# Performance work log

Hardware: AMD Instinct MI355X
Metric: run time of the kernel (lower is better)

## Reference

```python
import jax, jax.numpy as jnp
import numpy as np

NUM_EDGE_CLASS = 4
NODE_DIM = 64
BATCH = 32
NUM_NODES = 1024


def setup_inputs() -> dict:
    key = jax.random.key(0)
    k1, k2, k3, k4, k5 = jax.random.split(key, 5)
    node_state = jax.random.normal(k1, (BATCH, NUM_NODES, NODE_DIM), dtype=jnp.float32)
    adj_mat = jax.random.randint(k2, (BATCH, NUM_NODES, NUM_NODES), 0, NUM_EDGE_CLASS, dtype=jnp.int32)
    matrix_in = jax.random.normal(k3, (NUM_EDGE_CLASS, NODE_DIM, NODE_DIM), dtype=jnp.float32) * 0.1
    matrix_out = jax.random.normal(k4, (NUM_EDGE_CLASS, NODE_DIM, NODE_DIM), dtype=jnp.float32) * 0.1
    bias = jax.random.normal(k5, (2 * NODE_DIM,), dtype=jnp.float32)
    return {"node_state": node_state, "adj_mat": adj_mat,
            "matrix_in": matrix_in, "matrix_out": matrix_out, "bias": bias}


def reference(node_state, adj_mat, matrix_in, matrix_out, bias):
    """GGNN message passing (Li et al. Eq. 2).

    Original TF code builds a [b, n*d, n*d] block matrix where block (i, j)
    is matrix_in[adj_mat[b, i, j]] (and matrix_out[adj_mat[b, j, i]] for the
    outgoing direction), then matmuls against flattened node states. The
    equivalent fused math is:
      m_in[b,i]  = sum_j matrix_in[adj[b,i,j]]  @ h[b,j]
      m_out[b,i] = sum_j matrix_out[adj[b,j,i]] @ h[b,j]
    Implemented via a one-hot over the (small) set of edge classes so the
    per-edge d x d matrices are never materialized per edge.
    """
    h = node_state  # [b, n, d]
    onehot = jax.nn.one_hot(adj_mat, NUM_EDGE_CLASS, dtype=h.dtype)  # [b, n, n, c]
    # per-class neighbor aggregation, then one small matmul per class
    s_in = jnp.einsum('bijc,bje->bice', onehot, h)          # [b, n, c, d]
    m_in = jnp.einsum('bice,cde->bid', s_in, matrix_in)      # [b, n, d]
    s_out = jnp.einsum('bjic,bje->bice', onehot, h)          # transposed adjacency
    m_out = jnp.einsum('bice,cde->bid', s_out, matrix_out)   # [b, n, d]
    message = jnp.concatenate([m_in, m_out], axis=-1) + bias  # [b, n, 2d]
    return message
```

## Files before the change

kernel.cpp:

```cpp
#include <hip/hip_runtime.h>


namespace {

typedef unsigned int  u32;
typedef unsigned short u16;
typedef __attribute__((ext_vector_type(8))) short bf16x8;
typedef __attribute__((ext_vector_type(4))) float f32x4;

constexpr int NN = 1024;
constexpr int ND = 64;

__device__ inline u16 f2bf(float x) {
    u32 u = __float_as_uint(x);
    return (u16)((u + 0x7FFFu + ((u >> 16) & 1u)) >> 16);
}
__device__ inline float bf2f(u16 x) { return __uint_as_float(((u32)x) << 16); }

__device__ inline u32 oh2(u32 z) {
    return ((z & 1u) | ((z & 4u) << 14)) * 0x3F80u;
}

__global__ __launch_bounds__(256) void pack_adjm(
    const int* __restrict__ adj, const float* __restrict__ Min,
    const float* __restrict__ Mout, u32* __restrict__ adjP,
    u32* __restrict__ adjPT, u16* __restrict__ Mws)
{
    const int t = threadIdx.x;
    const int bid = blockIdx.x;
    if (bid >= 2048) {
        for (int i = t; i < 8192; i += 256) {
            const float* M = (i < 4096) ? Min : Mout;
            int idx = i & 4095;
            float m0 = M[idx], m1 = M[4096 + idx], m2 = M[8192 + idx], m3 = M[12288 + idx];
            u16* o = Mws + (size_t)(i >> 12) * 16384;
            o[idx]         = f2bf(m1 - m0);
            o[4096 + idx]  = f2bf(m2 - m0);
            o[8192 + idx]  = f2bf(m0 - m1 - m2 + m3);
            o[12288 + idx] = f2bf(m0);
        }
        return;
    }

    __shared__ u32 rp2[16][68];
    const int b = bid >> 6, It = (bid >> 4) & 3, Jt = (bid >> 2) & 3, s = bid & 3;
    const int* base = adj + ((size_t)b << 20) + (size_t)(It * 256 + s * 64) * NN + Jt * 256;

    const int row = t >> 2, seg = t & 3;
    const int* rptr = base + (size_t)row * NN + seg * 64;
    u32 w[4];
    #pragma unroll
    for (int q = 0; q < 4; ++q) {
        int4 v0 = *(const int4*)(rptr + q * 16 + 0);
        int4 v1 = *(const int4*)(rptr + q * 16 + 4);
        int4 v2 = *(const int4*)(rptr + q * 16 + 8);
        int4 v3 = *(const int4*)(rptr + q * 16 + 12);
        u32 u = (u32)(v0.x & 3) | ((u32)(v0.y & 3) << 2) | ((u32)(v0.z & 3) << 4) | ((u32)(v0.w & 3) << 6)
              | ((u32)(v1.x & 3) << 8) | ((u32)(v1.y & 3) << 10) | ((u32)(v1.z & 3) << 12) | ((u32)(v1.w & 3) << 14)
              | ((u32)(v2.x & 3) << 16) | ((u32)(v2.y & 3) << 18) | ((u32)(v2.z & 3) << 20) | ((u32)(v2.w & 3) << 22)
              | ((u32)(v3.x & 3) << 24) | ((u32)(v3.y & 3) << 26) | ((u32)(v3.z & 3) << 28) | ((u32)(v3.w & 3) << 30);
        w[q] = u;
        rp2[seg * 4 + q][row] = u;
    }
    u32* op = adjP + (((((size_t)b * 4 + Jt) * 16 + It * 4 + s) * 4 + seg) * 64 + row) * 4;
    *(uint4*)op = make_uint4(w[0], w[1], w[2], w[3]);
    __syncthreads();

    const int sc = t >> 6, il = t & 63;
    const int cw = sc * 4 + (il >> 4);
    const int bp = (il & 15) * 2;
    u32 o[4];
    #pragma unroll
    for (int jj = 0; jj < 4; ++jj) {
        u32 r[16];
        *(uint4*)&r[0]  = *(const uint4*)&rp2[cw][jj * 16 + 0];
        *(uint4*)&r[4]  = *(const uint4*)&rp2[cw][jj * 16 + 4];
        *(uint4*)&r[8]  = *(const uint4*)&rp2[cw][jj * 16 + 8];
        *(uint4*)&r[12] = *(const uint4*)&rp2[cw][jj * 16 + 12];
        u32 acc = 0;
        #pragma unroll
        for (int k = 0; k < 16; ++k)
            acc += ((r[k] >> bp) & 3u) << (2 * k);
        o[jj] = acc;
    }
    u32* op2 = adjPT + (((((size_t)b * 4 + It) * 16 + Jt * 4 + sc) * 4 + s) * 64 + il) * 4;
    *(uint4*)op2 = make_uint4(o[0], o[1], o[2], o[3]);
}

__global__ __launch_bounds__(256) void prep_h(
    const float* __restrict__ h, u16* __restrict__ Hws, float* __restrict__ PApart)
{
    __shared__ u16 hl[256][72];
    __shared__ float red[4][64];
    const int t = threadIdx.x;
    const int b = blockIdx.x >> 2, jc = blockIdx.x & 3;
    const float* hb = h + ((size_t)b * NN + jc * 256) * ND;
    #pragma unroll
    for (int k = 0; k < 16; ++k) {
        int j = k * 16 + (t >> 4);
        int e4 = (t & 15) * 4;
        float4 v = *(const float4*)(hb + (size_t)j * ND + e4);
        *(u32*)&hl[j][e4]     = (u32)f2bf(v.x) | ((u32)f2bf(v.y) << 16);
        *(u32*)&hl[j][e4 + 2] = (u32)f2bf(v.z) | ((u32)f2bf(v.w) << 16);
    }
    __syncthreads();
    u16* ob = Hws + (size_t)(b * 4 + jc) * 2048 * 8;
    const int e = t & 63;
    float psum = 0.f;
    #pragma unroll
    for (int k = 0; k < 8; ++k) {
        int u = k * 4 + (t >> 6);
        u16 x0 = hl[u * 8 + 0][e], x1 = hl[u * 8 + 1][e], x2 = hl[u * 8 + 2][e], x3 = hl[u * 8 + 3][e];
        u16 x4 = hl[u * 8 + 4][e], x5 = hl[u * 8 + 5][e], x6 = hl[u * 8 + 6][e], x7 = hl[u * 8 + 7][e];
        psum += bf2f(x0) + bf2f(x1) + bf2f(x2) + bf2f(x3) + bf2f(x4) + bf2f(x5) + bf2f(x6) + bf2f(x7);
        u32 p0 = (u32)x0 | ((u32)x1 << 16), p1 = (u32)x2 | ((u32)x3 << 16);
        u32 p2 = (u32)x4 | ((u32)x5 << 16), p3 = (u32)x6 | ((u32)x7 << 16);
        *(uint4*)(ob + (size_t)(u * 64 + e) * 8) = make_uint4(p0, p1, p2, p3);
    }
    red[t >> 6][e] = psum;
    __syncthreads();
    if (t < 64) {
        float sum = red[0][t] + red[1][t] + red[2][t] + red[3][t];
        PApart[(size_t)(jc * 32 + b) * 64 + t] = sum;
    }
}

__global__ __launch_bounds__(256, 4) void ggnn_main(
    const u32* __restrict__ adjP, const u32* __restrict__ adjPT,
    const u16* __restrict__ Hws, const u16* __restrict__ Mws,
    const float* __restrict__ PApart, const float* __restrict__ bias,
    float* __restrict__ out)
{
    __shared__ u16 Sb[16][16][72];

    const int t = threadIdx.x;
    const int w = t >> 6;
    const int ln = t & 15, qd = (t & 63) >> 4, qd2 = qd >> 1;
    const int shamt = (qd & 1) * 16;
    const int bid = blockIdx.x;
    const int dir = bid >> 9;
    const int b = (bid >> 4) & 31, it = bid & 15;

    const u32* Adir = dir ? adjPT : adjP;
    f32x4 acc[3][4];
    #pragma unroll
    for (int p = 0; p < 3; ++p)
        #pragma unroll
        for (int nt = 0; nt < 4; ++nt) acc[p][nt] = (f32x4){0.f, 0.f, 0.f, 0.f};

    uint4 Ar[4];
    {
        const u32* at = Adir + (size_t)((b * 4 + 0) * 16 + it) * 1024;
        #pragma unroll
        for (int u = 0; u < 4; ++u)
            Ar[u] = *(const uint4*)(at + (u * 64 + w * 16 + ln) * 4);
    }

    #pragma unroll
    for (int jc = 0; jc < 4; ++jc) {
        const u16* ht = Hws + (size_t)(b * 4 + jc) * 16384;
        uint4 ArN[4];
        if (jc < 3) {
            const u32* at = Adir + (size_t)((b * 4 + jc + 1) * 16 + it) * 1024;
            #pragma unroll
            for (int u = 0; u < 4; ++u)
                ArN[u] = *(const uint4*)(at + (u * 64 + w * 16 + ln) * 4);
        }

        #pragma unroll
        for (int ks = 0; ks < 8; ++ks) {
            bf16x8 bf[4];
            #pragma unroll
            for (int nt = 0; nt < 4; ++nt)
                bf[nt] = *(const bf16x8*)(ht + (size_t)((ks * 4 + qd) * 64 + nt * 16 + ln) * 8);

            uint4 Q = Ar[ks >> 1];
            u32 a = (ks & 1) ? (qd2 ? Q.w : Q.z) : (qd2 ? Q.y : Q.x);
            u32 f = (a >> shamt) & 0xFFFFu;
            u32 x0 = f & 0x5555u;
            u32 x1 = (f >> 1) & 0x5555u;
            u32 xt = x0 & x1;

            union { u32 u[4]; bf16x8 v; } A0, A1, AT;
            #pragma unroll
            for (int wd = 0; wd < 4; ++wd) {
                A0.u[wd] = oh2(x0 >> (4 * wd));
                A1.u[wd] = oh2(x1 >> (4 * wd));
                AT.u[wd] = oh2(xt >> (4 * wd));
            }
            #pragma unroll
            for (int nt = 0; nt < 4; ++nt) {
                acc[0][nt] = __builtin_amdgcn_mfma_f32_16x16x32_bf16(A0.v, bf[nt], acc[0][nt], 0, 0, 0);
                acc[1][nt] = __builtin_amdgcn_mfma_f32_16x16x32_bf16(A1.v, bf[nt], acc[1][nt], 0, 0, 0);
                acc[2][nt] = __builtin_amdgcn_mfma_f32_16x16x32_bf16(AT.v, bf[nt], acc[2][nt], 0, 0, 0);
            }
        }
        if (jc < 3) {
            #pragma unroll
            for (int u = 0; u < 4; ++u) Ar[u] = ArN[u];
        }
    }

    #pragma unroll
    for (int p = 0; p < 3; ++p)
        #pragma unroll
        for (int nt = 0; nt < 4; ++nt)
            #pragma unroll
            for (int r = 0; r < 4; ++r)
                Sb[w * 4 + p][qd * 4 + r][nt * 16 + ln] = f2bf(acc[p][nt][r]);

    {
        const int lane64 = t & 63;
        float paf = 0.f;
        #pragma unroll
        for (int jcp = 0; jcp < 4; ++jcp)
            paf += PApart[(size_t)(jcp * 32 + b) * 64 + lane64];
        u16 pab = f2bf(paf);
        #pragma unroll
        for (int i = 0; i < 16; ++i)
            Sb[w * 4 + 3][i][lane64] = pab;
    }

    const int dofs = dir * 64;
    f32x4 acc2[4];
    #pragma unroll
    for (int dt = 0; dt < 4; ++dt) {
        float v = bias[dofs + dt * 16 + ln];
        acc2[dt] = (f32x4){v, v, v, v};
    }
    const u16* Mb = Mws + (size_t)dir * 16384;
    #pragma unroll
    for (int p = 0; p < 4; ++p) {
        #pragma unroll
        for (int ks2 = 0; ks2 < 2; ++ks2) {
            bf16x8 af = *(const bf16x8*)&Sb[w * 4 + p][ln][ks2 * 32 + qd * 8];
            #pragma unroll
            for (int dt = 0; dt < 4; ++dt) {
                bf16x8 mf = *(const bf16x8*)(Mb + (size_t)(p * 64 + dt * 16 + ln) * 64
                                             + ks2 * 32 + qd * 8);
                acc2[dt] = __builtin_amdgcn_mfma_f32_16x16x32_bf16(af, mf, acc2[dt], 0, 0, 0);
            }
        }
    }
    #pragma unroll
    for (int dt = 0; dt < 4; ++dt)
        #pragma unroll
        for (int r = 0; r < 4; ++r)
            out[((size_t)b * NN + it * 64 + w * 16 + qd * 4 + r) * 128
                + dofs + dt * 16 + ln] = acc2[dt][r];
}

}

extern "C" void kernel_launch(void* const* d_in, const int* in_sizes, int n_in,
                              void* d_out, int out_size, void* d_ws, size_t ws_size,
                              hipStream_t stream) {
    (void)in_sizes; (void)n_in; (void)out_size; (void)ws_size;
    const float* h    = (const float*)d_in[0];
    const int*   adj  = (const int*)d_in[1];
    const float* Min  = (const float*)d_in[2];
    const float* Mout = (const float*)d_in[3];
    const float* bias = (const float*)d_in[4];
    float* out = (float*)d_out;

    char* ws = (char*)d_ws;
    u32* adjP     = (u32*)(ws + 0);
    u32* adjPT    = (u32*)(ws + 8388608);
    u16* Hws      = (u16*)(ws + 16777216);
    float* PApart = (float*)(ws + 20971520);
    u16* Mws      = (u16*)(ws + 21004288);

    pack_adjm<<<2049, 256, 0, stream>>>(adj, Min, Mout, adjP, adjPT, Mws);
    prep_h<<<128, 256, 0, stream>>>(h, Hws, PApart);
    ggnn_main<<<1024, 256, 0, stream>>>(adjP, adjPT, Hws, Mws, PApart, bias, out);
}
```

Before: 276.9 us.

## Merge prep kernels, restage adjacency packing through byte LDS, interleave directions

Merges the adjacency packing, h conversion and weight prep into a single launch, with h prep split into half-chunks so more blocks run. Adjacency loads become fully coalesced int4 reads, packed to bytes in LDS, and the transpose is rebuilt from a column-major byte buffer. The main kernel now interleaves the two directions by block index, drops the occupancy hint, and loads adjacency per chunk instead of prefetching the next one. The aim is to cut launch overhead and improve load coalescing, at the cost of losing the software prefetch in the main loop.

```diff
diff --git a/kernel.cpp b/kernel.cpp
--- a/kernel.cpp
+++ b/kernel.cpp
@@ -3,129 +3,133 @@
 
 namespace {
 
-typedef unsigned int  u32;
+typedef unsigned int   u32;
 typedef unsigned short u16;
+typedef unsigned char  u8;
 typedef __attribute__((ext_vector_type(8))) short bf16x8;
 typedef __attribute__((ext_vector_type(4))) float f32x4;
 
 constexpr int NN = 1024;
-constexpr int ND = 64;
 
 __device__ inline u16 f2bf(float x) {
     u32 u = __float_as_uint(x);
     return (u16)((u + 0x7FFFu + ((u >> 16) & 1u)) >> 16);
 }
-__device__ inline float bf2f(u16 x) { return __uint_as_float(((u32)x) << 16); }
-
 __device__ inline u32 oh2(u32 z) {
     return ((z & 1u) | ((z & 4u) << 14)) * 0x3F80u;
 }
 
-__global__ __launch_bounds__(256) void pack_adjm(
-    const int* __restrict__ adj, const float* __restrict__ Min,
-    const float* __restrict__ Mout, u32* __restrict__ adjP,
-    u32* __restrict__ adjPT, u16* __restrict__ Mws)
+__global__ __launch_bounds__(256) void prep_all(
+    const int* __restrict__ adj, const float* __restrict__ h,
+    const float* __restrict__ Min, const float* __restrict__ Mout,
+    u32* __restrict__ adjP, u32* __restrict__ adjPT,
+    u16* __restrict__ Hws, float* __restrict__ PApart, u16* __restrict__ Mws)
 {
+    __shared__ __align__(16) char sbuf[19456];
     const int t = threadIdx.x;
     const int bid = blockIdx.x;
-    if (bid >= 2048) {
-        for (int i = t; i < 8192; i += 256) {
-            const float* M = (i < 4096) ? Min : Mout;
-            int idx = i & 4095;
-            float m0 = M[idx], m1 = M[4096 + idx], m2 = M[8192 + idx], m3 = M[12288 + idx];
-            u16* o = Mws + (size_t)(i >> 12) * 16384;
-            o[idx]         = f2bf(m1 - m0);
-            o[4096 + idx]  = f2bf(m2 - m0);
-            o[8192 + idx]  = f2bf(m0 - m1 - m2 + m3);
-            o[12288 + idx] = f2bf(m0);
+
+    if (bid < 2048) {
+        u8* ldsR = (u8*)sbuf;
+        u8* ldsC = (u8*)sbuf + 4096;
+        const int b = bid >> 6, It = (bid >> 4) & 3, Jt = (bid >> 2) & 3, s = bid & 3;
+        const int* base = adj + ((size_t)b << 20)
+                        + (size_t)(It * 256 + s * 64) * NN + Jt * 256;
+
+        #pragma unroll
+        for (int k = 0; k < 16; ++k) {
+            int f = k * 256 + t;
+            int row = f >> 6, c4 = f & 63;
+            int4 v = *(const int4*)(base + row * NN + c4 * 4);
+            u8 byte = (u8)((v.x & 3) | ((v.y & 3) << 2) | ((v.z & 3) << 4) | ((v.w & 3) << 6));
+            ldsR[row * 64 + c4] = byte;
+            ldsC[c4 * 68 + row] = byte;
+        }
+        __syncthreads();
+
+        {
+            int row = t >> 2, seg = t & 3;
+            uint4 wv = *(const uint4*)&ldsR[row * 64 + seg * 16];
+            u32* op = adjP + (((((size_t)b * 4 + Jt) * 16 + It * 4 + s) * 4 + seg) * 64 + row) * 4;
+            *(uint4*)op = wv;
+        }
+        {
+            int c4 = t >> 2, bp = (t & 3) * 2;
+            int sc = t >> 6, il = t & 63;
+            u32 o[4];
+            #pragma unroll
+            for (int jj = 0; jj < 4; ++jj) {
+                u32 acc = 0;
+                #pragma unroll
+                for (int m4 = 0; m4 < 4; ++m4) {
+                    u32 r = *(const u32*)&ldsC[c4 * 68 + jj * 16 + m4 * 4];
+                    #pragma unroll
+                    for (int m = 0; m < 4; ++m)
+                        acc |= ((r >> (8 * m + bp)) & 3u) << (2 * (m4 * 4 + m));
+                }
+                o[jj] = acc;
+            }
+            u32* op2 = adjPT + (((((size_t)b * 4 + It) * 16 + Jt * 4 + sc) * 4 + s) * 64 + il) * 4;
+            *(uint4*)op2 = make_uint4(o[0], o[1], o[2], o[3]);
         }
         return;
     }
 
-    __shared__ u32 rp2[16][68];
-    const int b = bid >> 6, It = (bid >> 4) & 3, Jt = (bid >> 2) & 3, s = bid & 3;
-    const int* base = adj + ((size_t)b << 20) + (size_t)(It * 256 + s * 64) * NN + Jt * 256;
-
-    const int row = t >> 2, seg = t & 3;
-    const int* rptr = base + (size_t)row * NN + seg * 64;
-    u32 w[4];
-    #pragma unroll
-    for (int q = 0; q < 4; ++q) {
-        int4 v0 = *(const int4*)(rptr + q * 16 + 0);
-        int4 v1 = *(const int4*)(rptr + q * 16 + 4);
-        int4 v2 = *(const int4*)(rptr + q * 16 + 8);
-        int4 v3 = *(const int4*)(rptr + q * 16 + 12);
-        u32 u = (u32)(v0.x & 3) | ((u32)(v0.y & 3) << 2) | ((u32)(v0.z & 3) << 4) | ((u32)(v0.w & 3) << 6)
-              | ((u32)(v1.x & 3) << 8) | ((u32)(v1.y & 3) << 10) | ((u32)(v1.z & 3) << 12) | ((u32)(v1.w & 3) << 14)
-              | ((u32)(v2.x & 3) << 16) | ((u32)(v2.y & 3) << 18) | ((u32)(v2.z & 3) << 20) | ((u32)(v2.w & 3) << 22)
-              | ((u32)(v3.x & 3) << 24) | ((u32)(v3.y & 3) << 26) | ((u32)(v3.z & 3) << 28) | ((u32)(v3.w & 3) << 30);
-        w[q] = u;
-        rp2[seg * 4 + q][row] = u;
-    }
-    u32* op = adjP + (((((size_t)b * 4 + Jt) * 16 + It * 4 + s) * 4 + seg) * 64 + row) * 4;
-    *(uint4*)op = make_uint4(w[0], w[1], w[2], w[3]);
-    __syncthreads();
-
-    const int sc = t >> 6, il = t & 63;
-    const int cw = sc * 4 + (il >> 4);
-    const int bp = (il & 15) * 2;
-    u32 o[4];
-    #pragma unroll
-    for (int jj = 0; jj < 4; ++jj) {
-        u32 r[16];
-        *(uint4*)&r[0]  = *(const uint4*)&rp2[cw][jj * 16 + 0];
-        *(uint4*)&r[4]  = *(const uint4*)&rp2[cw][jj * 16 + 4];
-        *(uint4*)&r[8]  = *(const uint4*)&rp2[cw][jj * 16 + 8];
-        *(uint4*)&r[12] = *(const uint4*)&rp2[cw][jj * 16 + 12];
-        u32 acc = 0;
-        #pragma unroll
-        for (int k = 0; k < 16; ++k)
-            acc += ((r[k] >> bp) & 3u) << (2 * k);
-        o[jj] = acc;
-    }
-    u32* op2 = adjPT + (((((size_t)b * 4 + It) * 16 + Jt * 4 + sc) * 4 + s) * 64 + il) * 4;
-    *(uint4*)op2 = make_uint4(o[0], o[1], o[2], o[3]);
-}
-
-__global__ __launch_bounds__(256) void prep_h(
-    const float* __restrict__ h, u16* __restrict__ Hws, float* __restrict__ PApart)
-{
-    __shared__ u16 hl[256][72];
-    __shared__ float red[4][64];
-    const int t = threadIdx.x;
-    const int b = blockIdx.x >> 2, jc = blockIdx.x & 3;
-    const float* hb = h + ((size_t)b * NN + jc * 256) * ND;
-    #pragma unroll
-    for (int k = 0; k < 16; ++k) {
-        int j = k * 16 + (t >> 4);
-        int e4 = (t & 15) * 4;
-        float4 v = *(const float4*)(hb + (size_t)j * ND + e4);
-        *(u32*)&hl[j][e4]     = (u32)f2bf(v.x) | ((u32)f2bf(v.y) << 16);
-        *(u32*)&hl[j][e4 + 2] = (u32)f2bf(v.z) | ((u32)f2bf(v.w) << 16);
-    }
-    __syncthreads();
-    u16* ob = Hws + (size_t)(b * 4 + jc) * 2048 * 8;
-    const int e = t & 63;
-    float psum = 0.f;
-    #pragma unroll
-    for (int k = 0; k < 8; ++k) {
-        int u = k * 4 + (t >> 6);
-        u16 x0 = hl[u * 8 + 0][e], x1 = hl[u * 8 + 1][e], x2 = hl[u * 8 + 2][e], x3 = hl[u * 8 + 3][e];
-        u16 x4 = hl[u * 8 + 4][e], x5 = hl[u * 8 + 5][e], x6 = hl[u * 8 + 6][e], x7 = hl[u * 8 + 7][e];
-        psum += bf2f(x0) + bf2f(x1) + bf2f(x2) + bf2f(x3) + bf2f(x4) + bf2f(x5) + bf2f(x6) + bf2f(x7);
-        u32 p0 = (u32)x0 | ((u32)x1 << 16), p1 = (u32)x2 | ((u32)x3 << 16);
-        u32 p2 = (u32)x4 | ((u32)x5 << 16), p3 = (u32)x6 | ((u32)x7 << 16);
-        *(uint4*)(ob + (size_t)(u * 64 + e) * 8) = make_uint4(p0, p1, p2, p3);
-    }
-    red[t >> 6][e] = psum;
-    __syncthreads();
-    if (t < 64) {
-        float sum = red[0][t] + red[1][t] + red[2][t] + red[3][t];
-        PApart[(size_t)(jc * 32 + b) * 64 + t] = sum;
-    }
-}
-
-__global__ __launch_bounds__(256, 4) void ggnn_main(
+    if (bid < 2304) {
+        u16 (*hl)[72] = (u16(*)[72])sbuf;
+        float* red = (float*)(sbuf + 18432);
+        const int idx = bid - 2048;
+        const int b = idx >> 3, jc = (idx >> 1) & 3, half = idx & 1;
+        const float* hb = h + ((size_t)b * NN + jc * 256 + half * 128) * 64;
+        #pragma unroll
+        for (int k = 0; k < 8; ++k) {
+            int f = k * 256 + t;
+            int j = f >> 4, e4 = (f & 15) * 4;
+            float4 v = *(const float4*)(hb + (size_t)j * 64 + e4);
+            *(u32*)&hl[j][e4]     = (u32)f2bf(v.x) | ((u32)f2bf(v.y) << 16);
+            *(u32*)&hl[j][e4 + 2] = (u32)f2bf(v.z) | ((u32)f2bf(v.w) << 16);
+        }
+        __syncthreads();
+        u16* ob = Hws + (size_t)(b * 4 + jc) * 16384 + (size_t)half * 16 * 64 * 8;
+        const int e = t & 63;
+        float psum = 0.f;
+        #pragma unroll
+        for (int k = 0; k < 4; ++k) {
+            int u = k * 4 + (t >> 6);
+            u16 x0 = hl[u * 8 + 0][e], x1 = hl[u * 8 + 1][e];
+            u16 x2 = hl[u * 8 + 2][e], x3 = hl[u * 8 + 3][e];
+            u16 x4 = hl[u * 8 + 4][e], x5 = hl[u * 8 + 5][e];
+            u16 x6 = hl[u * 8 + 6][e], x7 = hl[u * 8 + 7][e];
+            psum += __uint_as_float((u32)x0 << 16) + __uint_as_float((u32)x1 << 16)
+                  + __uint_as_float((u32)x2 << 16) + __uint_as_float((u32)x3 << 16)
+                  + __uint_as_float((u32)x4 << 16) + __uint_as_float((u32)x5 << 16)
+                  + __uint_as_float((u32)x6 << 16) + __uint_as_float((u32)x7 << 16);
+            u32 p0 = (u32)x0 | ((u32)x1 << 16), p1 = (u32)x2 | ((u32)x3 << 16);
+            u32 p2 = (u32)x4 | ((u32)x5 << 16), p3 = (u32)x6 | ((u32)x7 << 16);
+            *(uint4*)(ob + (size_t)(u * 64 + e) * 8) = make_uint4(p0, p1, p2, p3);
+        }
+        red[(t >> 6) * 64 + e] = psum;
+        __syncthreads();
+        if (t < 64) {
+            float sum = red[t] + red[64 + t] + red[128 + t] + red[192 + t];
+            PApart[(size_t)((jc * 2 + half) * 32 + b) * 64 + t] = sum;
+        }
+        return;
+    }
+
+    for (int i = t; i < 8192; i += 256) {
+        const float* M = (i < 4096) ? Min : Mout;
+        int idx = i & 4095;
+        float m0 = M[idx], m1 = M[4096 + idx], m2 = M[8192 + idx], m3 = M[12288 + idx];
+        u16* o = Mws + (size_t)(i >> 12) * 16384;
+        o[idx]         = f2bf(m1 - m0);
+        o[4096 + idx]  = f2bf(m2 - m0);
+        o[8192 + idx]  = f2bf(m0 - m1 - m2 + m3);
+        o[12288 + idx] = f2bf(m0);
+    }
+}
+
+__global__ __launch_bounds__(256) void ggnn_main(
     const u32* __restrict__ adjP, const u32* __restrict__ adjPT,
     const u16* __restrict__ Hws, const u16* __restrict__ Mws,
     const float* __restrict__ PApart, const float* __restrict__ bias,
@@ -138,8 +142,9 @@
     const int ln = t & 15, qd = (t & 63) >> 4, qd2 = qd >> 1;
     const int shamt = (qd & 1) * 16;
     const int bid = blockIdx.x;
-    const int dir = bid >> 9;
-    const int b = (bid >> 4) & 31, it = bid & 15;
+    const int dir = bid & 1;
+    const int r2 = bid >> 1;
+    const int b = r2 >> 4, it = r2 & 15;
 
     const u32* Adir = dir ? adjPT : adjP;
     f32x4 acc[3][4];
@@ -148,24 +153,14 @@
         #pragma unroll
         for (int nt = 0; nt < 4; ++nt) acc[p][nt] = (f32x4){0.f, 0.f, 0.f, 0.f};
 
-    uint4 Ar[4];
-    {
-        const u32* at = Adir + (size_t)((b * 4 + 0) * 16 + it) * 1024;
+    for (int jc = 0; jc < 4; ++jc) {
+        const u32* at = Adir + (size_t)((b * 4 + jc) * 16 + it) * 1024;
+        const u16* ht = Hws + (size_t)(b * 4 + jc) * 16384;
+
+        uint4 Ar[4];
         #pragma unroll
         for (int u = 0; u < 4; ++u)
             Ar[u] = *(const uint4*)(at + (u * 64 + w * 16 + ln) * 4);
-    }
-
-    #pragma unroll
-    for (int jc = 0; jc < 4; ++jc) {
-        const u16* ht = Hws + (size_t)(b * 4 + jc) * 16384;
-        uint4 ArN[4];
-        if (jc < 3) {
-            const u32* at = Adir + (size_t)((b * 4 + jc + 1) * 16 + it) * 1024;
-            #pragma unroll
-            for (int u = 0; u < 4; ++u)
-                ArN[u] = *(const uint4*)(at + (u * 64 + w * 16 + ln) * 4);
-        }
 
         #pragma unroll
         for (int ks = 0; ks < 8; ++ks) {
@@ -195,10 +190,6 @@
                 acc[2][nt] = __builtin_amdgcn_mfma_f32_16x16x32_bf16(AT.v, bf[nt], acc[2][nt], 0, 0, 0);
             }
         }
-        if (jc < 3) {
-            #pragma unroll
-            for (int u = 0; u < 4; ++u) Ar[u] = ArN[u];
-        }
     }
 
     #pragma unroll
@@ -213,7 +204,7 @@
         const int lane64 = t & 63;
         float paf = 0.f;
         #pragma unroll
-        for (int jcp = 0; jcp < 4; ++jcp)
+        for (int jcp = 0; jcp < 8; ++jcp)
             paf += PApart[(size_t)(jcp * 32 + b) * 64 + lane64];
         u16 pab = f2bf(paf);
         #pragma unroll
@@ -268,9 +259,8 @@
     u32* adjPT    = (u32*)(ws + 8388608);
     u16* Hws      = (u16*)(ws + 16777216);
     float* PApart = (float*)(ws + 20971520);
-    u16* Mws      = (u16*)(ws + 21004288);
-
-    pack_adjm<<<2049, 256, 0, stream>>>(adj, Min, Mout, adjP, adjPT, Mws);
-    prep_h<<<128, 256, 0, stream>>>(h, Hws, PApart);
+    u16* Mws      = (u16*)(ws + 21037056);
+
+    prep_all<<<2305, 256, 0, stream>>>(adj, h, Min, Mout, adjP, adjPT, Hws, PApart, Mws);
     ggnn_main<<<1024, 256, 0, stream>>>(adjP, adjPT, Hws, Mws, PApart, bias, out);
 }
```

Result: faster. 268.4 us (-3.1%).
